# Kernel tuning notes

Hardware: AMD Instinct MI355X
Metric: run time of the kernel (lower is better)

## Reference

```python
import jax, jax.numpy as jnp
import numpy as np

G, IN_D, OUT_D, KQ_D = 8192, 512, 512, 128
EPS = 1e-12  # torch F.normalize default eps


def setup_inputs() -> dict:
    key = jax.random.key(0)
    ks = jax.random.split(key, 7)
    s_in = 1.0 / np.sqrt(IN_D)
    return {
        "x": jax.random.normal(ks[0], (G, IN_D), dtype=jnp.float32),
        "Wk": jax.random.uniform(ks[1], (KQ_D, IN_D), jnp.float32, -s_in, s_in),
        "bk": jax.random.uniform(ks[2], (KQ_D,), jnp.float32, -s_in, s_in),
        "Wq": jax.random.uniform(ks[3], (KQ_D, IN_D), jnp.float32, -s_in, s_in),
        "bq": jax.random.uniform(ks[4], (KQ_D,), jnp.float32, -s_in, s_in),
        "Wv": jax.random.uniform(ks[5], (OUT_D, IN_D), jnp.float32, -s_in, s_in),
        "bv": jax.random.uniform(ks[6], (OUT_D,), jnp.float32, -s_in, s_in),
    }


def reference(x, Wk, bk, Wq, bq, Wv, bv):
    # QKV projections (torch Linear: x @ W^T + b)
    k = x @ Wk.T + bk            # [g, kq]
    q = x @ Wq.T + bq            # [g, kq]
    v = x @ Wv.T + bv            # [g, outD]
    # g x g attention scores
    scores = k @ q.T             # [g, g]
    # L2-normalize each row (F.normalize with dim=-1): x / max(||x||_2, eps)
    norm = jnp.sqrt(jnp.sum(scores * scores, axis=-1, keepdims=True))
    scores_n = scores / jnp.maximum(norm, EPS)
    # value matmul + residual
    return scores_n @ v + v      # [g, outD]
```

## Files before the change

### kernel.cpp

```cpp
#include <hip/hip_runtime.h>
#include <hip/hip_bf16.h>
#include <stdint.h>

typedef __attribute__((ext_vector_type(8))) short bf16x8;
typedef __attribute__((ext_vector_type(4))) float f32x4;

__device__ __forceinline__ unsigned short f2bf(float f) {
  union { float f; uint32_t u; } v; v.f = f;
  uint32_t u = v.u;
  return (unsigned short)((u + 0x7fffu + ((u >> 16) & 1u)) >> 16);
}
__device__ __forceinline__ float bf2f(unsigned short h) {
  union { uint32_t u; float f; } v; v.u = ((uint32_t)h) << 16;
  return v.f;
}

#define GLL(g, l) __builtin_amdgcn_global_load_lds( \
    (const __attribute__((address_space(1))) void*)(g), \
    (__attribute__((address_space(3))) void*)(l), 16, 0, 0)
#define WAITV(N) asm volatile("s_waitcnt vmcnt(" #N ")" ::: "memory")
#define SFENCE() __builtin_amdgcn_sched_barrier(0)
#define RBAR()   __builtin_amdgcn_s_barrier()

__global__ void cvt_all(const float* __restrict__ x,
                        const float* __restrict__ wk, const float* __restrict__ wq,
                        const float* __restrict__ wv,
                        unsigned short* __restrict__ xb, unsigned short* __restrict__ wb) {
  const int i = (blockIdx.x * 256 + threadIdx.x) * 4;
  const float* src; unsigned short* dst; int off;
  if (i < 4194304) { src = x; dst = xb; off = i; }
  else {
    const int j = i - 4194304;
    if (j < 65536)       { src = wk; off = j; }
    else if (j < 131072) { src = wq; off = j - 65536; }
    else                 { src = wv; off = j - 131072; }
    dst = wb + (j - off);
  }
  const float4 v = *(const float4*)(src + off);
  ushort4 o; o.x = f2bf(v.x); o.y = f2bf(v.y); o.z = f2bf(v.z); o.w = f2bf(v.w);
  *(ushort4*)(dst + off) = o;
}

__global__ __launch_bounds__(256, 3) void qkv_gemm(
    const unsigned short* __restrict__ xb, const unsigned short* __restrict__ wb,
    const float* __restrict__ pbk, const float* __restrict__ pbq, const float* __restrict__ pbv,
    unsigned short* __restrict__ kb, unsigned short* __restrict__ qtb,
    unsigned short* __restrict__ vb, unsigned short* __restrict__ vtb)
{
  __shared__ unsigned short Alds[2][64 * 64];
  __shared__ unsigned short Blds[2][128 * 64];
  const int tid = threadIdx.x;
  const int lane = tid & 63;
  const int wid = tid >> 6;
  const int wm = wid >> 1, wn = wid & 1;
  const int wg = blockIdx.x;
  const int xcd = wg & 7, sl = wg >> 3;
  const int bx = xcd * 16 + sl / 6;
  const int by = sl % 6;
  const int m0 = bx * 64, n0 = by * 128;
  const int l15 = lane & 15, l4 = lane >> 4;

  f32x4 acc[2][4] = {};

  auto stage = [&](int b, int kt) {
    const int k0 = kt * 64;
    #pragma unroll
    for (int p = 0; p < 2; ++p) {
      const int e = p * 256 + tid;
      const int row = e >> 3;
      const int cs = (e & 7) ^ (row & 7);
      GLL(xb + (size_t)(m0 + row) * 512 + k0 + cs * 8, &Alds[b][(p * 256 + (tid & ~63)) * 8]);
    }
    #pragma unroll
    for (int p = 0; p < 4; ++p) {
      const int e = p * 256 + tid;
      const int row = e >> 3;
      const int cs = (e & 7) ^ (row & 7);
      GLL(wb + (size_t)(n0 + row) * 512 + k0 + cs * 8, &Blds[b][(p * 256 + (tid & ~63)) * 8]);
    }
  };

  stage(0, 0);
  stage(1, 1);

  for (int kt = 0; kt < 8; ++kt) {
    const int cur = kt & 1;
    if (kt < 7) { WAITV(6); } else { WAITV(0); }
    RBAR();
    SFENCE();
    #pragma unroll
    for (int kk = 0; kk < 2; ++kk) {
      bf16x8 af[2], bfv[4];
      #pragma unroll
      for (int i = 0; i < 2; ++i) {
        const int ra = wm * 32 + i * 16 + l15;
        const int c  = kk * 4 + l4;
        af[i] = *(const bf16x8*)(&Alds[cur][ra * 64 + ((c ^ (ra & 7)) * 8)]);
      }
      #pragma unroll
      for (int j = 0; j < 4; ++j) {
        const int rb = wn * 64 + j * 16 + l15;
        const int c  = kk * 4 + l4;
        bfv[j] = *(const bf16x8*)(&Blds[cur][rb * 64 + ((c ^ (rb & 7)) * 8)]);
      }
      #pragma unroll
      for (int i = 0; i < 2; ++i)
        #pragma unroll
        for (int j = 0; j < 4; ++j)
          acc[i][j] = __builtin_amdgcn_mfma_f32_16x16x32_bf16(af[i], bfv[j], acc[i][j], 0, 0, 0);
    }
    SFENCE();
    RBAR();
    if (kt < 6) stage(cur, kt + 2);
  }

  #pragma unroll
  for (int i = 0; i < 2; ++i) {
    #pragma unroll
    for (int j = 0; j < 4; ++j) {
      const int rbase = m0 + wm * 32 + i * 16 + l4 * 4;
      const int c = n0 + wn * 64 + j * 16 + l15;
      const float bias = (c < 128) ? pbk[c] : (c < 256) ? pbq[c - 128] : pbv[c - 256];
      unsigned short o[4];
      #pragma unroll
      for (int r = 0; r < 4; ++r) o[r] = f2bf(acc[i][j][r] + bias);
      if (c < 128) {
        #pragma unroll
        for (int r = 0; r < 4; ++r) kb[(size_t)(rbase + r) * 128 + c] = o[r];
      } else if (c < 256) {
        ushort4 t; t.x = o[0]; t.y = o[1]; t.z = o[2]; t.w = o[3];
        *(ushort4*)(qtb + (size_t)(c - 128) * 8192 + rbase) = t;
      } else {
        const int vcol = c - 256;
        #pragma unroll
        for (int r = 0; r < 4; ++r) vb[(size_t)(rbase + r) * 512 + vcol] = o[r];
        ushort4 t; t.x = o[0]; t.y = o[1]; t.z = o[2]; t.w = o[3];
        *(ushort4*)(vtb + (size_t)vcol * 8192 + rbase) = t;
      }
    }
  }
}

__global__ __launch_bounds__(512) void gh_gemm(
    const unsigned short* __restrict__ qtb, const unsigned short* __restrict__ vtb,
    unsigned short* __restrict__ pb)
{
  __shared__ unsigned short Alds[2][128 * 64];
  __shared__ unsigned short Blds[2][80 * 64];
  const int tid = threadIdx.x, lane = tid & 63, wid = tid >> 6;
  const int l15 = lane & 15, l4 = lane >> 4;
  const int kc = blockIdx.x, nq = blockIdx.y;
  const int g0 = kc * 256;
  const int m0 = wid * 16;

  f32x4 acc[5] = {};

  auto stage = [&](int b, int st) {
    const int gs = g0 + st * 64;
    #pragma unroll
    for (int p = 0; p < 2; ++p) {
      const int e = p * 512 + tid;
      const int row = e >> 3;
      const int cs = (e & 7) ^ (row & 7);
      GLL(qtb + (size_t)row * 8192 + gs + cs * 8, &Alds[b][(p * 512 + (tid & ~63)) * 8]);
    }
    {
      const int row = tid >> 3;
      const int cglob = nq * 80 + row;
      const unsigned short* src = (cglob < 128) ? (qtb + (size_t)cglob * 8192)
                                                : (vtb + (size_t)(cglob - 128) * 8192);
      const int cs = (tid & 7) ^ (row & 7);
      GLL(src + gs + cs * 8, &Blds[b][(tid & ~63) * 8]);
    }
    if (tid < 128) {
      const int e = 512 + tid;
      const int row = e >> 3;
      const int cglob = nq * 80 + row;
      const unsigned short* src = (cglob < 128) ? (qtb + (size_t)cglob * 8192)
                                                : (vtb + (size_t)(cglob - 128) * 8192);
      const int cs = (e & 7) ^ (row & 7);
      GLL(src + gs + cs * 8, &Blds[b][(512 + (tid & ~63)) * 8]);
    }
  };

  stage(0, 0);
  stage(1, 1);

  for (int st = 0; st < 4; ++st) {
    const int cur = st & 1;
    if (st < 3) { WAITV(3); } else { WAITV(0); }
    RBAR();
    SFENCE();
    #pragma unroll
    for (int ks = 0; ks < 2; ++ks) {
      const int ra = m0 + l15;
      const int ca = ks * 4 + l4;
      const bf16x8 af = *(const bf16x8*)(&Alds[cur][ra * 64 + ((ca ^ (ra & 7)) * 8)]);
      #pragma unroll
      for (int nf = 0; nf < 5; ++nf) {
        const int rb = nf * 16 + l15;
        const bf16x8 bf = *(const bf16x8*)(&Blds[cur][rb * 64 + ((ca ^ (rb & 7)) * 8)]);
        acc[nf] = __builtin_amdgcn_mfma_f32_16x16x32_bf16(af, bf, acc[nf], 0, 0, 0);
      }
    }
    SFENCE();
    RBAR();
    if (st < 2) stage(cur, st + 2);
  }

  #pragma unroll
  for (int nf = 0; nf < 5; ++nf) {
    const int col = nq * 80 + nf * 16 + l15;
    #pragma unroll
    for (int r = 0; r < 4; ++r) {
      const int row = m0 + l4 * 4 + r;
      pb[((size_t)kc * 128 + row) * 640 + col] = f2bf(acc[nf][r]);
    }
  }
}

__global__ void gh_finalize(const unsigned short* __restrict__ pb,
                            unsigned short* __restrict__ Gb, unsigned short* __restrict__ Hbt) {
  const int idx = blockIdx.x * 256 + threadIdx.x;
  float s = 0.f;
  #pragma unroll
  for (int p = 0; p < 32; ++p) s += bf2f(pb[(size_t)p * 81920 + idx]);
  const int m = idx / 640, c = idx % 640;
  if (c < 128) Gb[m * 128 + c] = f2bf(s);
  else         Hbt[(size_t)(c - 128) * 128 + m] = f2bf(s);
}

__global__ __launch_bounds__(512, 2) void tnorm(
    const unsigned short* __restrict__ kb, const unsigned short* __restrict__ Gb,
    float* __restrict__ rnm)
{
  __shared__ unsigned short Kld[128 * 128];
  __shared__ unsigned short Gld[128 * 128];
  const int tid = threadIdx.x, lane = tid & 63, wid = tid >> 6;
  const int l15 = lane & 15, l4 = lane >> 4;
  const int m0 = blockIdx.x * 128;

  #pragma unroll
  for (int p = 0; p < 4; ++p) {
    const int e = p * 512 + tid;
    const int row = e >> 4, ch = e & 15;
    const int cs = ch ^ ((row & 7) << 1);
    GLL(kb + (size_t)(m0 + row) * 128 + cs * 8, &Kld[(e & ~63) * 8]);
    GLL(Gb + (size_t)row * 128 + cs * 8,        &Gld[(e & ~63) * 8]);
  }
  WAITV(0);
  __syncthreads();

  bf16x8 af[4];
  #pragma unroll
  for (int ks = 0; ks < 4; ++ks) {
    const int row = wid * 16 + l15, ci = ks * 4 + l4;
    af[ks] = *(const bf16x8*)((const char*)Kld + row * 256 + ((ci ^ ((row & 7) << 1)) * 16));
  }
  f32x4 tac[8] = {};
  #pragma unroll
  for (int ks = 0; ks < 4; ++ks) {
    #pragma unroll
    for (int nf = 0; nf < 8; ++nf) {
      const int grow = nf * 16 + l15, ci = ks * 4 + l4;
      const bf16x8 bf = *(const bf16x8*)((const char*)Gld + grow * 256 +
                                         ((ci ^ ((grow & 7) << 1)) * 16));
      tac[nf] = __builtin_amdgcn_mfma_f32_16x16x32_bf16(af[ks], bf, tac[nf], 0, 0, 0);
    }
  }

  float ssq[4] = {0.f, 0.f, 0.f, 0.f};
  #pragma unroll
  for (int nf = 0; nf < 8; ++nf) {
    #pragma unroll
    for (int r = 0; r < 4; ++r) {
      const int row = wid * 16 + l4 * 4 + r;
      const int col = nf * 16 + l15;
      const unsigned short kv = *(const unsigned short*)((const char*)Kld + row * 256 +
          ((((col >> 3)) ^ ((row & 7) << 1)) * 16) + (col & 7) * 2);
      ssq[r] += tac[nf][r] * bf2f(kv);
    }
  }
  #pragma unroll
  for (int d = 1; d < 16; d <<= 1)
    #pragma unroll
    for (int r = 0; r < 4; ++r) ssq[r] += __shfl_xor(ssq[r], d);
  if (l15 == 0) {
    #pragma unroll
    for (int r = 0; r < 4; ++r)
      rnm[m0 + wid * 16 + l4 * 4 + r] = 1.0f / fmaxf(sqrtf(ssq[r]), 1e-12f);
  }
}

__global__ __launch_bounds__(512, 4) void uv_out(
    const unsigned short* __restrict__ kb, const unsigned short* __restrict__ Hbt,
    const float* __restrict__ rnm, const unsigned short* __restrict__ vb,
    float* __restrict__ out)
{
  __shared__ unsigned short Kld[128 * 128];
  __shared__ unsigned short Hld[128 * 128];
  const int tid = threadIdx.x, lane = tid & 63, wid = tid >> 6;
  const int l15 = lane & 15, l4 = lane >> 4;
  const int m0 = blockIdx.x * 128, n0 = blockIdx.y * 128;
  const int wm = wid >> 2, wn = wid & 3;

  #pragma unroll
  for (int p = 0; p < 4; ++p) {
    const int e = p * 512 + tid;
    const int row = e >> 4, ch = e & 15;
    const int cs = ch ^ ((row & 7) << 1);
    GLL(kb  + (size_t)(m0 + row) * 128 + cs * 8, &Kld[(e & ~63) * 8]);
    GLL(Hbt + (size_t)(n0 + row) * 128 + cs * 8, &Hld[(e & ~63) * 8]);
  }
  WAITV(0);
  __syncthreads();

  f32x4 acc[4][2] = {};
  #pragma unroll
  for (int ks = 0; ks < 4; ++ks) {
    const int ci = ks * 4 + l4;
    bf16x8 af[4], bf[2];
    #pragma unroll
    for (int i = 0; i < 4; ++i) {
      const int row = wm * 64 + i * 16 + l15;
      af[i] = *(const bf16x8*)((const char*)Kld + row * 256 + ((ci ^ ((row & 7) << 1)) * 16));
    }
    #pragma unroll
    for (int j = 0; j < 2; ++j) {
      const int col = wn * 32 + j * 16 + l15;
      bf[j] = *(const bf16x8*)((const char*)Hld + col * 256 + ((ci ^ ((col & 7) << 1)) * 16));
    }
    #pragma unroll
    for (int i = 0; i < 4; ++i)
      #pragma unroll
      for (int j = 0; j < 2; ++j)
        acc[i][j] = __builtin_amdgcn_mfma_f32_16x16x32_bf16(af[i], bf[j], acc[i][j], 0, 0, 0);
  }

  #pragma unroll
  for (int i = 0; i < 4; ++i) {
    float rn[4];
    #pragma unroll
    for (int r = 0; r < 4; ++r) rn[r] = rnm[m0 + wm * 64 + i * 16 + l4 * 4 + r];
    #pragma unroll
    for (int j = 0; j < 2; ++j) {
      const int col = n0 + wn * 32 + j * 16 + l15;
      #pragma unroll
      for (int r = 0; r < 4; ++r) {
        const int row = m0 + wm * 64 + i * 16 + l4 * 4 + r;
        out[(size_t)row * 512 + col] =
            acc[i][j][r] * rn[r] + bf2f(vb[(size_t)row * 512 + col]);
      }
    }
  }
}

extern "C" void kernel_launch(void* const* d_in, const int* in_sizes, int n_in,
                              void* d_out, int out_size, void* d_ws, size_t ws_size,
                              hipStream_t stream) {
  const float* x  = (const float*)d_in[0];
  const float* Wk = (const float*)d_in[1];
  const float* bk = (const float*)d_in[2];
  const float* Wq = (const float*)d_in[3];
  const float* bq = (const float*)d_in[4];
  const float* Wv = (const float*)d_in[5];
  const float* bv = (const float*)d_in[6];
  float* out = (float*)d_out;

  char* ws = (char*)d_ws;
  unsigned short* xb   = (unsigned short*)(ws);
  unsigned short* wb   = (unsigned short*)(ws + 8388608);
  unsigned short* kb   = (unsigned short*)(ws + 9175040);
  unsigned short* vb   = (unsigned short*)(ws + 11272192);
  unsigned short* vtb  = (unsigned short*)(ws + 19660800);
  unsigned short* qtb  = (unsigned short*)(ws + 28049408);
  unsigned short* pb   = (unsigned short*)(ws + 30146560);
  unsigned short* Gb   = (unsigned short*)(ws + 35389440);
  unsigned short* Hbt  = (unsigned short*)(ws + 35422208);
  float*          rnm  = (float*)(ws + 35553280);

  cvt_all<<<4480, 256, 0, stream>>>(x, Wk, Wq, Wv, xb, wb);
  qkv_gemm<<<768, 256, 0, stream>>>(xb, wb, bk, bq, bv, kb, qtb, vb, vtb);
  gh_gemm<<<dim3(32, 8), 512, 0, stream>>>(qtb, vtb, pb);
  gh_finalize<<<320, 256, 0, stream>>>(pb, Gb, Hbt);
  tnorm<<<64, 512, 0, stream>>>(kb, Gb, rnm);
  uv_out<<<dim3(64, 4), 512, 0, stream>>>(kb, Hbt, rnm, vb, out);
}
```

Baseline: 45.76 us.

## Fuse x fp32-to-bf16 conversion into QKV GEMM A-tile loading

The separate conversion pass over x is removed. The QKV GEMM now stages fp32 x tiles directly into LDS with an XOR swizzle and converts them to bf16 in registers using packed convert instructions before each MFMA. This drops one full read and write of the 8 MB bf16 copy of x and one kernel launch. In exchange the A tile doubles its LDS footprint, launch bounds drop from 3 to 2 blocks, and each A fragment needs extra LDS reads and conversion instructions.

After: 52.79 us. +15.4%, slower.

```diff
diff --git a/kernel.cpp b/kernel.cpp
--- a/kernel.cpp
+++ b/kernel.cpp
@@ -13,6 +13,14 @@
 __device__ __forceinline__ float bf2f(unsigned short h) {
   union { uint32_t u; float f; } v; v.u = ((uint32_t)h) << 16;
   return v.f;
+}
+__device__ __forceinline__ bf16x8 cvt8(f32x4 lo, f32x4 hi) {
+  union { bf16x8 v; uint32_t u[4]; } r;
+  asm("v_cvt_pk_bf16_f32 %0, %1, %2" : "=v"(r.u[0]) : "v"(lo[0]), "v"(lo[1]));
+  asm("v_cvt_pk_bf16_f32 %0, %1, %2" : "=v"(r.u[1]) : "v"(lo[2]), "v"(lo[3]));
+  asm("v_cvt_pk_bf16_f32 %0, %1, %2" : "=v"(r.u[2]) : "v"(hi[0]), "v"(hi[1]));
+  asm("v_cvt_pk_bf16_f32 %0, %1, %2" : "=v"(r.u[3]) : "v"(hi[2]), "v"(hi[3]));
+  return r.v;
 }
 
 #define GLL(g, l) __builtin_amdgcn_global_load_lds( \
@@ -22,32 +30,25 @@
 #define SFENCE() __builtin_amdgcn_sched_barrier(0)
 #define RBAR()   __builtin_amdgcn_s_barrier()
 
-__global__ void cvt_all(const float* __restrict__ x,
-                        const float* __restrict__ wk, const float* __restrict__ wq,
-                        const float* __restrict__ wv,
-                        unsigned short* __restrict__ xb, unsigned short* __restrict__ wb) {
+__global__ void cvt_w(const float* __restrict__ wk, const float* __restrict__ wq,
+                      const float* __restrict__ wv, unsigned short* __restrict__ wb) {
   const int i = (blockIdx.x * 256 + threadIdx.x) * 4;
-  const float* src; unsigned short* dst; int off;
-  if (i < 4194304) { src = x; dst = xb; off = i; }
-  else {
-    const int j = i - 4194304;
-    if (j < 65536)       { src = wk; off = j; }
-    else if (j < 131072) { src = wq; off = j - 65536; }
-    else                 { src = wv; off = j - 131072; }
-    dst = wb + (j - off);
-  }
+  const float* src; int off;
+  if (i < 65536)       { src = wk; off = i; }
+  else if (i < 131072) { src = wq; off = i - 65536; }
+  else                 { src = wv; off = i - 131072; }
   const float4 v = *(const float4*)(src + off);
   ushort4 o; o.x = f2bf(v.x); o.y = f2bf(v.y); o.z = f2bf(v.z); o.w = f2bf(v.w);
-  *(ushort4*)(dst + off) = o;
-}
-
-__global__ __launch_bounds__(256, 3) void qkv_gemm(
-    const unsigned short* __restrict__ xb, const unsigned short* __restrict__ wb,
+  *(ushort4*)(wb + i) = o;
+}
+
+__global__ __launch_bounds__(256, 2) void qkv_gemm(
+    const float* __restrict__ x, const unsigned short* __restrict__ wb,
     const float* __restrict__ pbk, const float* __restrict__ pbq, const float* __restrict__ pbv,
     unsigned short* __restrict__ kb, unsigned short* __restrict__ qtb,
     unsigned short* __restrict__ vb, unsigned short* __restrict__ vtb)
 {
-  __shared__ unsigned short Alds[2][64 * 64];
+  __shared__ float          A32[2][64 * 64];
   __shared__ unsigned short Blds[2][128 * 64];
   const int tid = threadIdx.x;
   const int lane = tid & 63;
@@ -65,11 +66,11 @@
   auto stage = [&](int b, int kt) {
     const int k0 = kt * 64;
     #pragma unroll
-    for (int p = 0; p < 2; ++p) {
+    for (int p = 0; p < 4; ++p) {
       const int e = p * 256 + tid;
-      const int row = e >> 3;
-      const int cs = (e & 7) ^ (row & 7);
-      GLL(xb + (size_t)(m0 + row) * 512 + k0 + cs * 8, &Alds[b][(p * 256 + (tid & ~63)) * 8]);
+      const int row = e >> 4;
+      const int cs = (e & 15) ^ (row & 15);
+      GLL(x + (size_t)(m0 + row) * 512 + k0 + cs * 4, &A32[b][(p * 256 + (tid & ~63)) * 4]);
     }
     #pragma unroll
     for (int p = 0; p < 4; ++p) {
@@ -85,22 +86,25 @@
 
   for (int kt = 0; kt < 8; ++kt) {
     const int cur = kt & 1;
-    if (kt < 7) { WAITV(6); } else { WAITV(0); }
+    if (kt < 7) { WAITV(8); } else { WAITV(0); }
     RBAR();
     SFENCE();
     #pragma unroll
     for (int kk = 0; kk < 2; ++kk) {
       bf16x8 af[2], bfv[4];
+      const int c = kk * 4 + l4;
       #pragma unroll
       for (int i = 0; i < 2; ++i) {
         const int ra = wm * 32 + i * 16 + l15;
-        const int c  = kk * 4 + l4;
-        af[i] = *(const bf16x8*)(&Alds[cur][ra * 64 + ((c ^ (ra & 7)) * 8)]);
+        const int s4 = ra & 15;
+        const char* rowp = (const char*)&A32[cur][0] + ra * 256;
+        const f32x4 lo = *(const f32x4*)(rowp + ((((c << 1))     ^ s4) << 4));
+        const f32x4 hi = *(const f32x4*)(rowp + ((((c << 1) | 1) ^ s4) << 4));
+        af[i] = cvt8(lo, hi);
       }
       #pragma unroll
       for (int j = 0; j < 4; ++j) {
         const int rb = wn * 64 + j * 16 + l15;
-        const int c  = kk * 4 + l4;
         bfv[j] = *(const bf16x8*)(&Blds[cur][rb * 64 + ((c ^ (rb & 7)) * 8)]);
       }
       #pragma unroll
@@ -368,7 +372,6 @@
   float* out = (float*)d_out;
 
   char* ws = (char*)d_ws;
-  unsigned short* xb   = (unsigned short*)(ws);
   unsigned short* wb   = (unsigned short*)(ws + 8388608);
   unsigned short* kb   = (unsigned short*)(ws + 9175040);
   unsigned short* vb   = (unsigned short*)(ws + 11272192);
@@ -379,8 +382,8 @@
   unsigned short* Hbt  = (unsigned short*)(ws + 35422208);
   float*          rnm  = (float*)(ws + 35553280);
 
-  cvt_all<<<4480, 256, 0, stream>>>(x, Wk, Wq, Wv, xb, wb);
-  qkv_gemm<<<768, 256, 0, stream>>>(xb, wb, bk, bq, bv, kb, qtb, vb, vtb);
+  cvt_w<<<384, 256, 0, stream>>>(Wk, Wq, Wv, wb);
+  qkv_gemm<<<768, 256, 0, stream>>>(x, wb, bk, bq, bv, kb, qtb, vb, vtb);
   gh_gemm<<<dim3(32, 8), 512, 0, stream>>>(qtb, vtb, pb);
   gh_finalize<<<320, 256, 0, stream>>>(pb, Gb, Hbt);
   tnorm<<<64, 512, 0, stream>>>(kb, Gb, rnm);
```
